# Optimization experiments

Measured on AMD Instinct MI355X. Metric: run time of the kernel, lower is better.

Reference implementation:

```python
import jax, jax.numpy as jnp
import numpy as np

B, S, DIM, H, HD = 4, 512, 1024, 16, 64
MAX_REL = 512           # max_relative_positions
SCALE_FACTOR = 3        # 1 + len(('c2p','p2c'))
SCORE_SCALE = (HD * SCALE_FACTOR) ** (-0.5)


def setup_inputs() -> dict:
    key = jax.random.key(0)
    ks = jax.random.split(key, 8)
    s = DIM ** -0.5
    return {
        "x": jax.random.normal(ks[0], (B, S, DIM), jnp.float32),
        "rel_embeddings": jax.random.normal(ks[1], (2 * MAX_REL, DIM), jnp.float32),
        "Wq": jax.random.normal(ks[2], (DIM, DIM), jnp.float32) * s,
        "bq": jnp.zeros((DIM,), jnp.float32),
        "Wk": jax.random.normal(ks[3], (DIM, DIM), jnp.float32) * s,
        "bk": jnp.zeros((DIM,), jnp.float32),
        "Wv": jax.random.normal(ks[4], (DIM, DIM), jnp.float32) * s,
        "bv": jnp.zeros((DIM,), jnp.float32),
    }


def _shape(t):
    # (B, S, DIM) -> (B, H, S, HD)
    return t.reshape(t.shape[0], -1, H, HD).transpose(0, 2, 1, 3)


def reference(x, rel_embeddings, Wq, bq, Wk, bk, Wv, bv):
    q = _shape(x @ Wq + bq)   # [B,H,S,HD]
    k = _shape(x @ Wk + bk)
    v = _shape(x @ Wv + bv)

    # relative positions: rel[i,j] = i - j (no bucketing since position_buckets=-1)
    ids = jnp.arange(S)
    rel_pos = ids[:, None] - ids[None, :]          # [S,S]
    att_span = S
    rel = rel_embeddings[MAX_REL - att_span:MAX_REL + att_span]  # [2S, DIM]

    idx = jnp.clip(rel_pos + att_span - 1, 0, 2 * att_span - 1)  # [S,S] in [0,2S-1]

    # c2p: query against projected relative-key embeddings, then gather over r
    pos_k = (rel @ Wk + bk).reshape(-1, H, HD)     # [2S,H,HD]
    c2p = jnp.einsum('bhqd,rhd->bhqr', q, pos_k)   # [B,H,S,2S]
    c2p = jnp.take_along_axis(c2p, jnp.broadcast_to(idx[None, None], (B, H, S, S)), axis=-1)

    # p2c: key against projected relative-query embeddings, gather, transpose
    pos_q = (rel @ Wq + bq).reshape(-1, H, HD)     # [2S,H,HD]
    p2c = jnp.einsum('bhkd,rhd->bhkr', k, pos_q)   # [B,H,S,2S]
    p2c = jnp.take_along_axis(p2c, jnp.broadcast_to(idx[None, None], (B, H, S, S)), axis=-1)
    p2c = jnp.swapaxes(p2c, -1, -2)

    bias = (c2p + p2c) * SCORE_SCALE               # [B,H,S,S]

    scores = jnp.einsum('bhqd,bhkd->bhqk', q, k) * SCORE_SCALE + bias
    probs = jax.nn.softmax(scores, axis=-1)        # dropout = identity (eval)
    out = jnp.einsum('bhqk,bhkd->bhqd', probs, v)  # [B,H,S,HD]
    out = out.transpose(0, 2, 1, 3).reshape(B, S, DIM)
    return out
```

## Files before the change

### kernel.cpp

```cpp
#include <hip/hip_runtime.h>
#include <math.h>

#define DIM_ 1024
#define B_ 4
#define S_ 512
#define H_ 16
#define HD_ 64
#define SCORE_SCALE_ 0.07216878364870323f

typedef __attribute__((ext_vector_type(8))) short bf16x8;
typedef __attribute__((ext_vector_type(4))) float f32x4;

__device__ __forceinline__ unsigned short f2bf(float f) {
    unsigned int u = __float_as_uint(f);
    u = u + 0x7fffu + ((u >> 16) & 1u);
    return (unsigned short)(u >> 16);
}
__device__ __forceinline__ float bfs(unsigned short s) { return __uint_as_float(((unsigned int)s) << 16); }

__device__ __forceinline__ void gload16(const void* g, void* l) {
    __builtin_amdgcn_global_load_lds((const __attribute__((address_space(1))) void*)g,
                                     (__attribute__((address_space(3))) void*)l, 16, 0, 0);
}

__global__ __launch_bounds__(256) void cvt2_bf16(const float* __restrict__ x,
                                                 const float* __restrict__ rel,
                                                 unsigned short* __restrict__ dst) {
    const int i = blockIdx.x * 256 + threadIdx.x;
    const float* src = (i < 524288) ? &x[(size_t)i * 4]
                                    : &rel[(size_t)(i - 524288) * 4];
    const float4 v = *(const float4*)src;
    ushort4 o;
    o.x = f2bf(v.x); o.y = f2bf(v.y); o.z = f2bf(v.z); o.w = f2bf(v.w);
    *(ushort4*)&dst[(size_t)i * 4] = o;
}

__global__ __launch_bounds__(256) void wtrans(
    const float* __restrict__ W0, const float* __restrict__ W1, const float* __restrict__ W2,
    unsigned short* __restrict__ T0, unsigned short* __restrict__ T1, unsigned short* __restrict__ T2)
{
    const float* __restrict__ W = blockIdx.z == 0 ? W0 : blockIdx.z == 1 ? W1 : W2;
    unsigned short* __restrict__ T = blockIdx.z == 0 ? T0 : blockIdx.z == 1 ? T1 : T2;
    __shared__ float tile[32][33];
    const int t = threadIdx.x;
    const int n0 = blockIdx.x * 32, k0 = blockIdx.y * 32;
    const int r = t >> 3, c4 = (t & 7) * 4;
    const float4 v = *(const float4*)&W[(size_t)(k0 + r) * DIM_ + n0 + c4];
    tile[r][c4 + 0] = v.x; tile[r][c4 + 1] = v.y; tile[r][c4 + 2] = v.z; tile[r][c4 + 3] = v.w;
    __syncthreads();
    ushort4 o;
    o.x = f2bf(tile[c4 + 0][r]); o.y = f2bf(tile[c4 + 1][r]);
    o.z = f2bf(tile[c4 + 2][r]); o.w = f2bf(tile[c4 + 3][r]);
    *(ushort4*)&T[(size_t)(n0 + r) * DIM_ + k0 + c4] = o;
}

__global__ __launch_bounds__(256) void gemm_mfma_bt(
    const unsigned short* __restrict__ Ab,
    const unsigned short* __restrict__ Wt0, const unsigned short* __restrict__ Wt1, const unsigned short* __restrict__ Wt2,
    const float* __restrict__ b0, const float* __restrict__ b1, const float* __restrict__ b2,
    unsigned short* __restrict__ C0, unsigned short* __restrict__ C1, unsigned short* __restrict__ C2)
{
    const int z = blockIdx.z;
    const int m0 = blockIdx.y * 128, n0 = blockIdx.x * 128;
    if (z == 2 && m0 >= 2048) return;
    const unsigned short* __restrict__ Wt = z == 0 ? Wt0 : z == 1 ? Wt1 : Wt2;
    const float* __restrict__ bias        = z == 0 ? b0  : z == 1 ? b1  : b2;
    unsigned short* __restrict__ C        = z == 0 ? C0  : z == 1 ? C1  : C2;
    const float scl = (z == 0) ? SCORE_SCALE_ : 1.0f;

    __shared__ unsigned short As[2][128 * 32];
    __shared__ unsigned short Bs[2][128 * 32];

    const int t = threadIdx.x, lane = t & 63, wave = t >> 6;
    const int wm = wave >> 1, wn = wave & 1;

    f32x4 acc[4][4];
#pragma unroll
    for (int i = 0; i < 4; ++i)
#pragma unroll
        for (int j = 0; j < 4; ++j) acc[i][j] = (f32x4){0.f, 0.f, 0.f, 0.f};

    const int c1 = wave * 64 + lane, c2 = c1 + 256;
    const int ar1 = c1 >> 2, ao1 = (c1 & 3) * 8;
    const int ar2 = c2 >> 2, ao2 = (c2 & 3) * 8;
    const int lr = lane & 15, lk = (lane >> 4) * 8;

#define STAGE(buf, kt) { \
    gload16(&Ab[(size_t)(m0 + ar1) * DIM_ + (kt) + ao1], &As[buf][c1 * 8]); \
    gload16(&Ab[(size_t)(m0 + ar2) * DIM_ + (kt) + ao2], &As[buf][c2 * 8]); \
    gload16(&Wt[(size_t)(n0 + ar1) * DIM_ + (kt) + ao1], &Bs[buf][c1 * 8]); \
    gload16(&Wt[(size_t)(n0 + ar2) * DIM_ + (kt) + ao2], &Bs[buf][c2 * 8]); }

    STAGE(0, 0)
    asm volatile("s_waitcnt vmcnt(0)" ::: "memory");
    __syncthreads();

    int cur = 0;
    for (int kt = 0; kt < DIM_; kt += 32) {
        if (kt + 32 < DIM_) STAGE(cur ^ 1, kt + 32)
        bf16x8 af[4], bfr[4];
#pragma unroll
        for (int i = 0; i < 4; ++i) {
            af[i]  = *(const bf16x8*)&As[cur][(wm * 64 + i * 16 + lr) * 32 + lk];
            bfr[i] = *(const bf16x8*)&Bs[cur][(wn * 64 + i * 16 + lr) * 32 + lk];
        }
#pragma unroll
        for (int i = 0; i < 4; ++i)
#pragma unroll
            for (int j = 0; j < 4; ++j)
                acc[i][j] = __builtin_amdgcn_mfma_f32_16x16x32_bf16(af[i], bfr[j], acc[i][j], 0, 0, 0);
        asm volatile("s_waitcnt vmcnt(0)" ::: "memory");
        __syncthreads();
        cur ^= 1;
    }
#undef STAGE

    const int rb = (lane >> 4) * 4;
#pragma unroll
    for (int j = 0; j < 4; ++j) {
        const int col = n0 + wn * 64 + j * 16 + lr;
        const float bv = bias[col];
#pragma unroll
        for (int i = 0; i < 4; ++i) {
            const int row = m0 + wm * 64 + i * 16 + rb;
#pragma unroll
            for (int r = 0; r < 4; ++r)
                C[(size_t)(row + r) * DIM_ + col] = f2bf((acc[i][j][r] + bv) * scl);
        }
    }
}

__global__ __launch_bounds__(256) void vtrans(const unsigned short* __restrict__ V,
                                              unsigned short* __restrict__ Vt) {
    const int t = threadIdx.x;
    const int k0 = blockIdx.x * 64;
    const int bh = blockIdx.y;
    const int b = bh >> 4, h = bh & 15;
    __shared__ unsigned short tl[64 * 72];
#pragma unroll
    for (int p = 0; p < 2; ++p) {
        const int idx = t + p * 256;
        const int r = idx >> 3, c8 = (idx & 7) * 8;
        const uint4 v = *(const uint4*)&V[((size_t)b * S_ + k0 + r) * DIM_ + h * HD_ + c8];
        *(uint4*)&tl[r * 72 + c8] = v;
    }
    __syncthreads();
#pragma unroll
    for (int p = 0; p < 2; ++p) {
        const int idx = t + p * 256;
        const int d = idx >> 3, k8 = (idx & 7) * 8;
        unsigned short tmp[8];
#pragma unroll
        for (int j = 0; j < 8; ++j) tmp[j] = tl[(k8 + j) * 72 + d];
        *(uint4*)&Vt[((size_t)bh * HD_ + d) * S_ + k0 + k8] = *(uint4*)tmp;
    }
}

__global__ __launch_bounds__(256) void fused_attn(
    const unsigned short* __restrict__ Q, const unsigned short* __restrict__ K,
    const unsigned short* __restrict__ Vt,
    const unsigned short* __restrict__ PK, const unsigned short* __restrict__ PQ,
    float* __restrict__ out)
{
    const int t = threadIdx.x, lane = t & 63, wave = t >> 6;
    const int lr = lane & 15, lg = lane >> 4;
    const int bh = blockIdx.x;
    const int q0 = blockIdx.y * 64;
    const int b = bh >> 4, h = bh & 15;
    const size_t base  = (size_t)b * S_ * DIM_ + h * HD_;
    const size_t vbase = (size_t)bh * HD_ * S_;

    __shared__ unsigned short K_lds[64 * 64];
    __shared__ unsigned short PK_lds[128 * 64];
    __shared__ unsigned short PQ_lds[128 * 64];
    __shared__ float Sb[64 * 65];
    __shared__ unsigned short P_lds[64 * 72];

    auto stage_tile = [&](int kn) {
        const int rbG_ = q0 - kn + 448;
        const int rbH_ = kn - q0 + 448;
#pragma unroll
        for (int p = 0; p < 2; ++p) {
            const int c = wave * 64 + lane + p * 256, r = c >> 3;
            const int jc = (c & 7) ^ (r & 7);
            gload16(&K[base + (size_t)(kn + r) * DIM_ + jc * 8], &K_lds[(size_t)c * 8]);
        }
#pragma unroll
        for (int p = 0; p < 4; ++p) {
            const int c = wave * 64 + lane + p * 256, r = c >> 3;
            const int jc = (c & 7) ^ (r & 7);
            gload16(&PK[(size_t)(rbG_ + r) * DIM_ + h * HD_ + jc * 8], &PK_lds[(size_t)c * 8]);
            gload16(&PQ[(size_t)(rbH_ + r) * DIM_ + h * HD_ + jc * 8], &PQ_lds[(size_t)c * 8]);
        }
    };

    bf16x8 af_q[2];
    {
        const int qrow = q0 + wave * 16 + lr;
        af_q[0] = *(const bf16x8*)&Q[base + (size_t)qrow * DIM_ + lg * 8];
        af_q[1] = *(const bf16x8*)&Q[base + (size_t)qrow * DIM_ + 32 + lg * 8];
    }

    f32x4 O_acc[4];
#pragma unroll
    for (int df = 0; df < 4; ++df) O_acc[df] = (f32x4){0.f, 0.f, 0.f, 0.f};
    float m_run[4], l_run[4];
#pragma unroll
    for (int r = 0; r < 4; ++r) { m_run[r] = -1e30f; l_run[r] = 0.f; }

    const int lqr = wave * 16 + lg * 4;
    const int swz = lr & 7;
    const int dbase = lg * 4 + 63 - lr;

    stage_tile(0);

    for (int k0 = 0; k0 < S_; k0 += 64) {
        asm volatile("s_waitcnt vmcnt(0)" ::: "memory");
        __syncthreads();

        f32x4 S_acc[4];
#pragma unroll
        for (int sf = 0; sf < 4; ++sf) S_acc[sf] = (f32x4){0.f, 0.f, 0.f, 0.f};
#pragma unroll
        for (int ks = 0; ks < 2; ++ks)
#pragma unroll
            for (int sf = 0; sf < 4; ++sf) {
                const bf16x8 bk = *(const bf16x8*)
                    &K_lds[(size_t)(sf * 16 + lr) * 64 + (((ks * 4 + lg) ^ swz) * 8)];
                S_acc[sf] = __builtin_amdgcn_mfma_f32_16x16x32_bf16(af_q[ks], bk, S_acc[sf], 0, 0, 0);
            }

        f32x4 G[5];
#pragma unroll
        for (int c = 0; c < 5; ++c) G[c] = (f32x4){0.f, 0.f, 0.f, 0.f};
#pragma unroll
        for (int ks = 0; ks < 2; ++ks)
#pragma unroll
            for (int c = 0; c < 5; ++c) {
                const bf16x8 bp = *(const bf16x8*)
                    &PK_lds[(size_t)((wave + c) * 16 + lr) * 64 + (((ks * 4 + lg) ^ swz) * 8)];
                G[c] = __builtin_amdgcn_mfma_f32_16x16x32_bf16(af_q[ks], bp, G[c], 0, 0, 0);
            }

        bf16x8 af_k[2];
#pragma unroll
        for (int ks = 0; ks < 2; ++ks)
            af_k[ks] = *(const bf16x8*)
                &K_lds[(size_t)(wave * 16 + lr) * 64 + (((ks * 4 + lg) ^ swz) * 8)];
        f32x4 Hf[5];
#pragma unroll
        for (int c = 0; c < 5; ++c) Hf[c] = (f32x4){0.f, 0.f, 0.f, 0.f};
#pragma unroll
        for (int ks = 0; ks < 2; ++ks)
#pragma unroll
            for (int c = 0; c < 5; ++c) {
                const bf16x8 bp = *(const bf16x8*)
                    &PQ_lds[(size_t)((wave + c) * 16 + lr) * 64 + (((ks * 4 + lg) ^ swz) * 8)];
                Hf[c] = __builtin_amdgcn_mfma_f32_16x16x32_bf16(af_k[ks], bp, Hf[c], 0, 0, 0);
            }

#pragma unroll
        for (int c = 0; c < 5; ++c)
#pragma unroll
            for (int reg = 0; reg < 4; ++reg) {
                const int lk = dbase + reg - 16 * c;
                if ((unsigned)lk < 64u) Sb[(lqr + reg) * 65 + lk] = G[c][reg];
            }
        __syncthreads();

#pragma unroll
        for (int c = 0; c < 5; ++c)
#pragma unroll
            for (int reg = 0; reg < 4; ++reg) {
                const int lq = dbase + reg - 16 * c;
                if ((unsigned)lq < 64u) Sb[lq * 65 + lqr + reg] += Hf[c][reg];
            }
        __syncthreads();

        bf16x8 vt[8];
#pragma unroll
        for (int ks = 0; ks < 2; ++ks)
#pragma unroll
            for (int df = 0; df < 4; ++df)
                vt[ks * 4 + df] = *(const bf16x8*)
                    &Vt[vbase + (size_t)(df * 16 + lr) * S_ + k0 + ks * 32 + lg * 8];

        float sv[16];
#pragma unroll
        for (int sf = 0; sf < 4; ++sf)
#pragma unroll
            for (int reg = 0; reg < 4; ++reg)
                sv[sf * 4 + reg] = S_acc[sf][reg] + Sb[(lqr + reg) * 65 + sf * 16 + lr];

        float mt[4];
#pragma unroll
        for (int reg = 0; reg < 4; ++reg)
            mt[reg] = fmaxf(fmaxf(sv[reg], sv[4 + reg]), fmaxf(sv[8 + reg], sv[12 + reg]));
#pragma unroll
        for (int off = 8; off >= 1; off >>= 1)
#pragma unroll
            for (int reg = 0; reg < 4; ++reg)
                mt[reg] = fmaxf(mt[reg], __shfl_xor(mt[reg], off));

        float al[4], rs[4];
#pragma unroll
        for (int reg = 0; reg < 4; ++reg) {
            const float mn = fmaxf(m_run[reg], mt[reg]);
            al[reg] = __expf(m_run[reg] - mn);
            m_run[reg] = mn;
            rs[reg] = 0.f;
        }
        unsigned short pb[16];
#pragma unroll
        for (int sf = 0; sf < 4; ++sf)
#pragma unroll
            for (int reg = 0; reg < 4; ++reg) {
                const float p = __expf(sv[sf * 4 + reg] - m_run[reg]);
                const unsigned short pr = f2bf(p);
                pb[sf * 4 + reg] = pr;
                rs[reg] += bfs(pr);
            }
#pragma unroll
        for (int off = 8; off >= 1; off >>= 1)
#pragma unroll
            for (int reg = 0; reg < 4; ++reg)
                rs[reg] += __shfl_xor(rs[reg], off);
#pragma unroll
        for (int reg = 0; reg < 4; ++reg)
            l_run[reg] = l_run[reg] * al[reg] + rs[reg];
#pragma unroll
        for (int df = 0; df < 4; ++df)
#pragma unroll
            for (int reg = 0; reg < 4; ++reg)
                O_acc[df][reg] *= al[reg];

#pragma unroll
        for (int sf = 0; sf < 4; ++sf)
#pragma unroll
            for (int reg = 0; reg < 4; ++reg)
                P_lds[(lqr + reg) * 72 + sf * 16 + lr] = pb[sf * 4 + reg];

#pragma unroll
        for (int ks = 0; ks < 2; ++ks) {
            const bf16x8 ap = *(const bf16x8*)&P_lds[(wave * 16 + lr) * 72 + ks * 32 + lg * 8];
#pragma unroll
            for (int df = 0; df < 4; ++df)
                O_acc[df] = __builtin_amdgcn_mfma_f32_16x16x32_bf16(ap, vt[ks * 4 + df], O_acc[df], 0, 0, 0);
        }

        if (k0 + 64 < S_) stage_tile(k0 + 64);
    }

#pragma unroll
    for (int df = 0; df < 4; ++df)
#pragma unroll
        for (int reg = 0; reg < 4; ++reg)
            out[((size_t)b * S_ + q0 + wave * 16 + lg * 4 + reg) * DIM_ +
                h * HD_ + df * 16 + lr] = O_acc[df][reg] / l_run[reg];
}

extern "C" void kernel_launch(void* const* d_in, const int* in_sizes, int n_in,
                              void* d_out, int out_size, void* d_ws, size_t ws_size,
                              hipStream_t stream) {
    (void)in_sizes; (void)n_in; (void)out_size; (void)ws_size;
    const float* x   = (const float*)d_in[0];
    const float* rel = (const float*)d_in[1];
    const float* Wq  = (const float*)d_in[2];
    const float* bq  = (const float*)d_in[3];
    const float* Wk  = (const float*)d_in[4];
    const float* bk  = (const float*)d_in[5];
    const float* Wv  = (const float*)d_in[6];
    const float* bv  = (const float*)d_in[7];
    float* out = (float*)d_out;

    unsigned short* Ab  = (unsigned short*)d_ws;
    unsigned short* Wtq = Ab  + (size_t)3072 * 1024;
    unsigned short* Wtk = Wtq + (size_t)1024 * 1024;
    unsigned short* Wtv = Wtk + (size_t)1024 * 1024;
    unsigned short* Cq  = Wtv + (size_t)1024 * 1024;
    unsigned short* Ck  = Cq  + (size_t)3072 * 1024;
    unsigned short* Cv  = Ck  + (size_t)3072 * 1024;
    unsigned short* Vtb = Cv  + (size_t)2048 * 1024;

    cvt2_bf16<<<3072, 256, 0, stream>>>(x, rel, Ab);
    wtrans<<<dim3(32, 32, 3), 256, 0, stream>>>(Wq, Wk, Wv, Wtq, Wtk, Wtv);
    gemm_mfma_bt<<<dim3(8, 24, 3), 256, 0, stream>>>(Ab, Wtq, Wtk, Wtv, bq, bk, bv, Cq, Ck, Cv);
    vtrans<<<dim3(8, 64), 256, 0, stream>>>(Cv, Vtb);

    const unsigned short* PKp = Ck + (size_t)2048 * 1024;
    const unsigned short* PQp = Cq + (size_t)2048 * 1024;

    fused_attn<<<dim3(64, 8), 256, 0, stream>>>(Cq, Ck, Vtb, PKp, PQp, out);
}
```

Before: 81.05 us.

## Merge prep kernels, compact GEMM grid, prefetch next K/V tile earlier

Merges the bf16 conversion and weight-transpose kernels into one launch, which removes one launch overhead and its gap. It also flattens the GEMM grid to 512 blocks so the early-exit blocks for the V projection are never launched. In the attention loop, the V^T register loads now happen earlier and the next tile's staging starts right after the first barrier, overlapping global loads with the bias and softmax work. The earlier staging must not overwrite LDS that is still being read (K/PK/PQ are done by then), and holding the loads longer may raise register pressure.

```diff
diff --git a/kernel.cpp b/kernel.cpp
--- a/kernel.cpp
+++ b/kernel.cpp
@@ -23,27 +23,30 @@
                                      (__attribute__((address_space(3))) void*)l, 16, 0, 0);
 }
 
-__global__ __launch_bounds__(256) void cvt2_bf16(const float* __restrict__ x,
-                                                 const float* __restrict__ rel,
-                                                 unsigned short* __restrict__ dst) {
-    const int i = blockIdx.x * 256 + threadIdx.x;
-    const float* src = (i < 524288) ? &x[(size_t)i * 4]
-                                    : &rel[(size_t)(i - 524288) * 4];
-    const float4 v = *(const float4*)src;
-    ushort4 o;
-    o.x = f2bf(v.x); o.y = f2bf(v.y); o.z = f2bf(v.z); o.w = f2bf(v.w);
-    *(ushort4*)&dst[(size_t)i * 4] = o;
-}
-
-__global__ __launch_bounds__(256) void wtrans(
+__global__ __launch_bounds__(256) void prep(
+    const float* __restrict__ x, const float* __restrict__ rel,
+    unsigned short* __restrict__ Ab,
     const float* __restrict__ W0, const float* __restrict__ W1, const float* __restrict__ W2,
     unsigned short* __restrict__ T0, unsigned short* __restrict__ T1, unsigned short* __restrict__ T2)
 {
-    const float* __restrict__ W = blockIdx.z == 0 ? W0 : blockIdx.z == 1 ? W1 : W2;
-    unsigned short* __restrict__ T = blockIdx.z == 0 ? T0 : blockIdx.z == 1 ? T1 : T2;
     __shared__ float tile[32][33];
+    const int bid = blockIdx.x;
     const int t = threadIdx.x;
-    const int n0 = blockIdx.x * 32, k0 = blockIdx.y * 32;
+    if (bid < 3072) {
+        const int i = bid * 256 + t;
+        const float* src = (i < 524288) ? &x[(size_t)i * 4]
+                                        : &rel[(size_t)(i - 524288) * 4];
+        const float4 v = *(const float4*)src;
+        ushort4 o;
+        o.x = f2bf(v.x); o.y = f2bf(v.y); o.z = f2bf(v.z); o.w = f2bf(v.w);
+        *(ushort4*)&Ab[(size_t)i * 4] = o;
+        return;
+    }
+    const int b2 = bid - 3072;
+    const int z = b2 >> 10, rem = b2 & 1023;
+    const float* __restrict__ W = z == 0 ? W0 : z == 1 ? W1 : W2;
+    unsigned short* __restrict__ T = z == 0 ? T0 : z == 1 ? T1 : T2;
+    const int n0 = (rem & 31) * 32, k0 = (rem >> 5) * 32;
     const int r = t >> 3, c4 = (t & 7) * 4;
     const float4 v = *(const float4*)&W[(size_t)(k0 + r) * DIM_ + n0 + c4];
     tile[r][c4 + 0] = v.x; tile[r][c4 + 1] = v.y; tile[r][c4 + 2] = v.z; tile[r][c4 + 3] = v.w;
@@ -60,9 +63,12 @@
     const float* __restrict__ b0, const float* __restrict__ b1, const float* __restrict__ b2,
     unsigned short* __restrict__ C0, unsigned short* __restrict__ C1, unsigned short* __restrict__ C2)
 {
-    const int z = blockIdx.z;
-    const int m0 = blockIdx.y * 128, n0 = blockIdx.x * 128;
-    if (z == 2 && m0 >= 2048) return;
+    const int gid = blockIdx.x;
+    int z, l;
+    if (gid < 192)      { z = 0; l = gid; }
+    else if (gid < 384) { z = 1; l = gid - 192; }
+    else                { z = 2; l = gid - 384; }
+    const int n0 = (l & 7) * 128, m0 = (l >> 3) * 128;
     const unsigned short* __restrict__ Wt = z == 0 ? Wt0 : z == 1 ? Wt1 : Wt2;
     const float* __restrict__ bias        = z == 0 ? b0  : z == 1 ? b1  : b2;
     unsigned short* __restrict__ C        = z == 0 ? C0  : z == 1 ? C1  : C2;
@@ -230,6 +236,14 @@
                 S_acc[sf] = __builtin_amdgcn_mfma_f32_16x16x32_bf16(af_q[ks], bk, S_acc[sf], 0, 0, 0);
             }
 
+        bf16x8 vt[8];
+#pragma unroll
+        for (int ks = 0; ks < 2; ++ks)
+#pragma unroll
+            for (int df = 0; df < 4; ++df)
+                vt[ks * 4 + df] = *(const bf16x8*)
+                    &Vt[vbase + (size_t)(df * 16 + lr) * S_ + k0 + ks * 32 + lg * 8];
+
         f32x4 G[5];
 #pragma unroll
         for (int c = 0; c < 5; ++c) G[c] = (f32x4){0.f, 0.f, 0.f, 0.f};
@@ -268,6 +282,8 @@
             }
         __syncthreads();
 
+        if (k0 + 64 < S_) stage_tile(k0 + 64);
+
 #pragma unroll
         for (int c = 0; c < 5; ++c)
 #pragma unroll
@@ -276,14 +292,6 @@
                 if ((unsigned)lq < 64u) Sb[lq * 65 + lqr + reg] += Hf[c][reg];
             }
         __syncthreads();
-
-        bf16x8 vt[8];
-#pragma unroll
-        for (int ks = 0; ks < 2; ++ks)
-#pragma unroll
-            for (int df = 0; df < 4; ++df)
-                vt[ks * 4 + df] = *(const bf16x8*)
-                    &Vt[vbase + (size_t)(df * 16 + lr) * S_ + k0 + ks * 32 + lg * 8];
 
         float sv[16];
 #pragma unroll
@@ -347,8 +355,6 @@
             for (int df = 0; df < 4; ++df)
                 O_acc[df] = __builtin_amdgcn_mfma_f32_16x16x32_bf16(ap, vt[ks * 4 + df], O_acc[df], 0, 0, 0);
         }
-
-        if (k0 + 64 < S_) stage_tile(k0 + 64);
     }
 
 #pragma unroll
@@ -382,9 +388,8 @@
     unsigned short* Cv  = Ck  + (size_t)3072 * 1024;
     unsigned short* Vtb = Cv  + (size_t)2048 * 1024;
 
-    cvt2_bf16<<<3072, 256, 0, stream>>>(x, rel, Ab);
-    wtrans<<<dim3(32, 32, 3), 256, 0, stream>>>(Wq, Wk, Wv, Wtq, Wtk, Wtv);
-    gemm_mfma_bt<<<dim3(8, 24, 3), 256, 0, stream>>>(Ab, Wtq, Wtk, Wtv, bq, bk, bv, Cq, Ck, Cv);
+    prep<<<6144, 256, 0, stream>>>(x, rel, Ab, Wq, Wk, Wv, Wtq, Wtk, Wtv);
+    gemm_mfma_bt<<<512, 256, 0, stream>>>(Ab, Wtq, Wtk, Wtv, bq, bk, bv, Cq, Ck, Cv);
     vtrans<<<dim3(8, 64), 256, 0, stream>>>(Cv, Vtb);
 
     const unsigned short* PKp = Ck + (size_t)2048 * 1024;
```

Result: no change. 81.26 us (+0.3%).
